# Kernel tuning notes

Hardware: AMD Instinct MI355X
Metric: run time of the kernel (lower is better)

Reference implementation:

```python
import jax, jax.numpy as jnp
import numpy as np

B, S, HID = 1, 2048, 4096
NH, NKV, HD = 32, 8, 128          # num_heads, num_key_value_heads, head_dim
N_REP = NH // NKV                  # GQA group size
ROPE_BASE = 10000.0


def rotate_half(x):
    x1, x2 = jnp.split(x, 2, axis=-1)
    return jnp.concatenate([-x2, x1], axis=-1)


def setup_inputs() -> dict:
    key = jax.random.key(0)
    k_hs, k_q, k_k, k_v, k_o = jax.random.split(key, 5)
    hidden_states = jax.random.normal(k_hs, (B, S, HID), dtype=jnp.float32)
    scale = 0.02
    wq = jax.random.normal(k_q, (HID, NH * HD), dtype=jnp.float32) * scale
    wk = jax.random.normal(k_k, (HID, NKV * HD), dtype=jnp.float32) * scale
    wv = jax.random.normal(k_v, (HID, NKV * HD), dtype=jnp.float32) * scale
    wo = jax.random.normal(k_o, (NH * HD, HID), dtype=jnp.float32) * scale
    # additive causal mask, 0 on/below diagonal, large negative above
    causal = jnp.tril(jnp.ones((S, S), dtype=bool))
    attention_mask = jnp.where(causal, 0.0, -1e9).astype(jnp.float32)[None, None]
    # RoPE cos/sin cache (LlamaRotaryEmbedding)
    inv_freq = 1.0 / (ROPE_BASE ** (jnp.arange(0, HD, 2, dtype=jnp.float32) / HD))
    t = jnp.arange(S, dtype=jnp.float32)
    freqs = jnp.outer(t, inv_freq)                 # [S, HD/2]
    emb = jnp.concatenate([freqs, freqs], axis=-1)  # [S, HD]
    cos, sin = jnp.cos(emb), jnp.sin(emb)
    return {"hidden_states": hidden_states, "attention_mask": attention_mask,
            "wq": wq, "wk": wk, "wv": wv, "wo": wo, "cos": cos, "sin": sin}


def reference(hidden_states, attention_mask, wq, wk, wv, wo, cos, sin):
    b, s, _ = hidden_states.shape
    # projections -> [b, heads, s, head_dim]
    q = (hidden_states @ wq).reshape(b, s, NH, HD).transpose(0, 2, 1, 3)
    k = (hidden_states @ wk).reshape(b, s, NKV, HD).transpose(0, 2, 1, 3)
    v = (hidden_states @ wv).reshape(b, s, NKV, HD).transpose(0, 2, 1, 3)
    # RoPE: cos/sin [s, hd] broadcast over batch and heads
    c = cos[None, None, :, :]
    sn = sin[None, None, :, :]
    q = q * c + rotate_half(q) * sn
    k = k * c + rotate_half(k) * sn
    # GQA repeat_kv: [b, nkv, s, d] -> [b, nh, s, d]
    k = jnp.repeat(k, N_REP, axis=1)
    v = jnp.repeat(v, N_REP, axis=1)
    scores = jnp.einsum('bhqd,bhkd->bhqk', q, k) / jnp.sqrt(jnp.float32(HD))
    scores = scores + attention_mask
    attn = jax.nn.softmax(scores.astype(jnp.float32), axis=-1).astype(q.dtype)
    out = jnp.einsum('bhqk,bhkd->bhqd', attn, v)        # [b, nh, s, d]
    out = out.transpose(0, 2, 1, 3).reshape(b, s, NH * HD)
    return out @ wo
```

## Files before the change

### kernel.cpp

```cpp
#include <hip/hip_runtime.h>


typedef __bf16 bf16_t;
typedef bf16_t bf16x8_t __attribute__((ext_vector_type(8)));
typedef float f32x4_t __attribute__((ext_vector_type(4)));

#define S_LEN 2048
#define HID 4096
#define NH 32
#define NKV 8
#define HD 128
#define KV_DIM 1024
#define QKV_DIM 6144
#define SCALE 0.08838834764831845f

__device__ __align__(16) bf16_t g_hsb[(size_t)S_LEN * HID];
__device__ __align__(16) bf16_t g_wqkvT[(size_t)QKV_DIM * HID];
__device__ __align__(16) bf16_t g_woT[(size_t)HID * HID];
__device__ __align__(16) bf16_t g_qkv[(size_t)S_LEN * QKV_DIM];
__device__ __align__(16) bf16_t g_vT[(size_t)NKV * HD * S_LEN];
__device__ __align__(16) bf16_t g_ao[(size_t)S_LEN * HID];

__device__ __forceinline__ void gl_lds16(const bf16_t* g, bf16_t* l) {
  __builtin_amdgcn_global_load_lds(
      (const __attribute__((address_space(1))) void*)g,
      (__attribute__((address_space(3))) void*)l, 16, 0, 0);
}

__global__ __launch_bounds__(256) void cast_f32_bf16(
    const float* __restrict__ in, bf16_t* __restrict__ out)
{
  size_t i = ((size_t)blockIdx.x * 256 + threadIdx.x) * 8;
  float4 a = *(const float4*)(in + i);
  float4 b = *(const float4*)(in + i + 4);
  bf16x8_t r;
  r[0] = (bf16_t)a.x; r[1] = (bf16_t)a.y; r[2] = (bf16_t)a.z; r[3] = (bf16_t)a.w;
  r[4] = (bf16_t)b.x; r[5] = (bf16_t)b.y; r[6] = (bf16_t)b.z; r[7] = (bf16_t)b.w;
  *(bf16x8_t*)(out + i) = r;
}

__global__ __launch_bounds__(256) void transpose_f32_bf16(
    const float* __restrict__ in, bf16_t* __restrict__ out, int is, int os)
{
  __shared__ __align__(16) bf16_t T[64 * 72];
  int r0 = blockIdx.x * 64, c0 = blockIdx.y * 64;
  int t = threadIdx.x;
#pragma unroll
  for (int it = 0; it < 2; ++it) {
    int idx = t + it * 256;
    int r = idx >> 3, c8 = (idx & 7) * 8;
    const float* p = in + (size_t)(r0 + r) * is + c0 + c8;
    float4 a = *(const float4*)p;
    float4 b = *(const float4*)(p + 4);
    bf16x8_t x;
    x[0] = (bf16_t)a.x; x[1] = (bf16_t)a.y; x[2] = (bf16_t)a.z; x[3] = (bf16_t)a.w;
    x[4] = (bf16_t)b.x; x[5] = (bf16_t)b.y; x[6] = (bf16_t)b.z; x[7] = (bf16_t)b.w;
    *(bf16x8_t*)(T + r * 72 + c8) = x;
  }
  __syncthreads();
#pragma unroll
  for (int it = 0; it < 2; ++it) {
    int idx = t + it * 256;
    int c = idx >> 3, r8 = (idx & 7) * 8;
    bf16x8_t x;
#pragma unroll
    for (int i = 0; i < 8; ++i) x[i] = T[(r8 + i) * 72 + c];
    *(bf16x8_t*)(out + (size_t)(c0 + c) * os + r0 + r8) = x;
  }
}

__global__ __launch_bounds__(256) void transpose_bf16(
    const bf16_t* __restrict__ in, bf16_t* __restrict__ out,
    int is, int os, int in_b, int out_b)
{
  __shared__ __align__(16) bf16_t T[64 * 72];
  const bf16_t* inp = in + (size_t)blockIdx.z * in_b;
  bf16_t* outp = out + (size_t)blockIdx.z * out_b;
  int r0 = blockIdx.x * 64, c0 = blockIdx.y * 64;
  int t = threadIdx.x;
#pragma unroll
  for (int it = 0; it < 2; ++it) {
    int idx = t + it * 256;
    int r = idx >> 3, c8 = (idx & 7) * 8;
    *(bf16x8_t*)(T + r * 72 + c8) =
        *(const bf16x8_t*)(inp + (size_t)(r0 + r) * is + c0 + c8);
  }
  __syncthreads();
#pragma unroll
  for (int it = 0; it < 2; ++it) {
    int idx = t + it * 256;
    int c = idx >> 3, r8 = (idx & 7) * 8;
    bf16x8_t x;
#pragma unroll
    for (int i = 0; i < 8; ++i) x[i] = T[(r8 + i) * 72 + c];
    *(bf16x8_t*)(outp + (size_t)(c0 + c) * os + r0 + r8) = x;
  }
}

template <typename CT>
__global__ __launch_bounds__(256) void gemm128(
    const bf16_t* __restrict__ A, const bf16_t* __restrict__ Bt,
    CT* __restrict__ C, int K, int N)
{
  __shared__ __align__(16) bf16_t As[128 * 32];
  __shared__ __align__(16) bf16_t Bs[128 * 32];
  int t = threadIdx.x;
  int wave = t >> 6, lane = t & 63, ln = lane & 15, lq = lane >> 4;
  int m0 = blockIdx.x * 128, n0 = blockIdx.y * 128;
  int wm = (wave >> 1) * 64, wn = (wave & 1) * 64;
  int srow = wave * 16 + (lane >> 2);
  int skc = (lane & 3) * 8;
  const bf16_t* Ag0 = A + (size_t)(m0 + srow) * K + skc;
  const bf16_t* Ag1 = A + (size_t)(m0 + 64 + srow) * K + skc;
  const bf16_t* Bg0 = Bt + (size_t)(n0 + srow) * K + skc;
  const bf16_t* Bg1 = Bt + (size_t)(n0 + 64 + srow) * K + skc;
  bf16_t* Al0 = As + (wave * 16) * 32;
  bf16_t* Al1 = As + (64 + wave * 16) * 32;
  bf16_t* Bl0 = Bs + (wave * 16) * 32;
  bf16_t* Bl1 = Bs + (64 + wave * 16) * 32;
  f32x4_t acc[4][4] = {};
  for (int k0 = 0; k0 < K; k0 += 32) {
    __syncthreads();
    gl_lds16(Ag0 + k0, Al0);
    gl_lds16(Ag1 + k0, Al1);
    gl_lds16(Bg0 + k0, Bl0);
    gl_lds16(Bg1 + k0, Bl1);
    __syncthreads();
    bf16x8_t af[4], bfr[4];
#pragma unroll
    for (int i = 0; i < 4; ++i) {
      af[i]  = *(const bf16x8_t*)(As + (wm + i * 16 + ln) * 32 + lq * 8);
      bfr[i] = *(const bf16x8_t*)(Bs + (wn + i * 16 + ln) * 32 + lq * 8);
    }
#pragma unroll
    for (int mt = 0; mt < 4; ++mt)
#pragma unroll
      for (int nt = 0; nt < 4; ++nt)
        acc[mt][nt] = __builtin_amdgcn_mfma_f32_16x16x32_bf16(
            af[mt], bfr[nt], acc[mt][nt], 0, 0, 0);
  }
#pragma unroll
  for (int mt = 0; mt < 4; ++mt)
#pragma unroll
    for (int nt = 0; nt < 4; ++nt)
#pragma unroll
      for (int r = 0; r < 4; ++r)
        C[(size_t)(m0 + wm + mt * 16 + lq * 4 + r) * N + n0 + wn + nt * 16 + ln] =
            (CT)acc[mt][nt][r];
}

__global__ __launch_bounds__(256) void rope_kernel(
    bf16_t* __restrict__ qkv, const float* __restrict__ cs,
    const float* __restrict__ sn)
{
  int idx = blockIdx.x * 256 + threadIdx.x;
  int d = idx & 63;
  int h = (idx >> 6) % (NH + NKV);
  int s = idx / (64 * (NH + NKV));
  float c = cs[s * HD + d], si = sn[s * HD + d];
  bf16_t* base = qkv + (size_t)s * QKV_DIM +
                 ((h < NH) ? h * HD : HID + (h - NH) * HD);
  float x1 = (float)base[d], x2 = (float)base[d + 64];
  base[d]      = (bf16_t)(x1 * c - x2 * si);
  base[d + 64] = (bf16_t)(x2 * c + x1 * si);
}

__global__ __launch_bounds__(256) void attn_kernel(
    const bf16_t* __restrict__ QKV, const bf16_t* __restrict__ VT,
    bf16_t* __restrict__ O)
{
  __shared__ __align__(16) bf16_t Ks[64 * 136];
  __shared__ __align__(16) bf16_t Vs[128 * 72];
  __shared__ __align__(16) bf16_t Ps[4 * 16 * 72];
  int t = threadIdx.x, wave = t >> 6, lane = t & 63;
  int ln = lane & 15, lq = lane >> 4;
  int bid = blockIdx.x;
  int qb = (S_LEN / 64 - 1) - (bid >> 5);
  int head = bid & 31, kvh = head >> 2;
  int q0 = qb * 64;
  int qr = q0 + wave * 16 + ln;

  bf16x8_t qf[4];
#pragma unroll
  for (int kk = 0; kk < 4; ++kk)
    qf[kk] = *(const bf16x8_t*)(QKV + (size_t)qr * QKV_DIM + head * HD +
                                kk * 32 + lq * 8);

  f32x4_t oa[8] = {};
  float m_r[4] = {-1e30f, -1e30f, -1e30f, -1e30f};
  float l_r[4] = {0.f, 0.f, 0.f, 0.f};

  int krow = t >> 4, kdc = (t & 15) * 8;
  int vrow = t >> 3, vkc = (t & 7) * 8;
  const bf16_t* Kg = QKV + HID + (size_t)kvh * HD;
  const bf16_t* Vg = VT + (size_t)kvh * HD * S_LEN;

  for (int kt = 0; kt <= qb; ++kt) {
    int kb = kt * 64;
    __syncthreads();
#pragma unroll
    for (int p = 0; p < 4; ++p) {
      int r_ = p * 16 + krow;
      *(bf16x8_t*)(Ks + r_ * 136 + kdc) =
          *(const bf16x8_t*)(Kg + (size_t)(kb + r_) * QKV_DIM + kdc);
      int d_ = p * 32 + vrow;
      *(bf16x8_t*)(Vs + d_ * 72 + vkc) =
          *(const bf16x8_t*)(Vg + (size_t)d_ * S_LEN + kb + vkc);
    }
    __syncthreads();

    f32x4_t sv[4] = {};
#pragma unroll
    for (int nt = 0; nt < 4; ++nt)
#pragma unroll
      for (int kk = 0; kk < 4; ++kk) {
        bf16x8_t kf = *(const bf16x8_t*)(Ks + (nt * 16 + ln) * 136 +
                                         kk * 32 + lq * 8);
        sv[nt] = __builtin_amdgcn_mfma_f32_16x16x32_bf16(qf[kk], kf, sv[nt],
                                                         0, 0, 0);
      }

    float p_[4][4];
    if (kt == qb) {
#pragma unroll
      for (int nt = 0; nt < 4; ++nt)
#pragma unroll
        for (int r = 0; r < 4; ++r) {
          int rq = wave * 16 + lq * 4 + r;
          p_[nt][r] = (nt * 16 + ln <= rq) ? sv[nt][r] * SCALE : -1e30f;
        }
    } else {
#pragma unroll
      for (int nt = 0; nt < 4; ++nt)
#pragma unroll
        for (int r = 0; r < 4; ++r) p_[nt][r] = sv[nt][r] * SCALE;
    }

    float mx[4];
#pragma unroll
    for (int r = 0; r < 4; ++r)
      mx[r] = fmaxf(fmaxf(p_[0][r], p_[1][r]), fmaxf(p_[2][r], p_[3][r]));
#pragma unroll
    for (int off = 8; off >= 1; off >>= 1)
#pragma unroll
      for (int r = 0; r < 4; ++r) mx[r] = fmaxf(mx[r], __shfl_xor(mx[r], off, 64));

    float al[4], rs[4];
#pragma unroll
    for (int r = 0; r < 4; ++r) {
      float mn = fmaxf(m_r[r], mx[r]);
      al[r] = __expf(m_r[r] - mn);
      m_r[r] = mn;
      rs[r] = 0.f;
#pragma unroll
      for (int nt = 0; nt < 4; ++nt) {
        p_[nt][r] = __expf(p_[nt][r] - mn);
        rs[r] += p_[nt][r];
      }
    }
#pragma unroll
    for (int off = 8; off >= 1; off >>= 1)
#pragma unroll
      for (int r = 0; r < 4; ++r) rs[r] += __shfl_xor(rs[r], off, 64);
#pragma unroll
    for (int r = 0; r < 4; ++r) l_r[r] = l_r[r] * al[r] + rs[r];
#pragma unroll
    for (int dt = 0; dt < 8; ++dt)
#pragma unroll
      for (int r = 0; r < 4; ++r) oa[dt][r] *= al[r];

    bf16_t* myP = Ps + wave * 16 * 72;
#pragma unroll
    for (int nt = 0; nt < 4; ++nt)
#pragma unroll
      for (int r = 0; r < 4; ++r)
        myP[(lq * 4 + r) * 72 + nt * 16 + ln] = (bf16_t)p_[nt][r];
    bf16x8_t pf0 = *(const bf16x8_t*)(myP + ln * 72 + lq * 8);
    bf16x8_t pf1 = *(const bf16x8_t*)(myP + ln * 72 + 32 + lq * 8);
#pragma unroll
    for (int dt = 0; dt < 8; ++dt) {
      bf16x8_t v0 = *(const bf16x8_t*)(Vs + (dt * 16 + ln) * 72 + lq * 8);
      bf16x8_t v1 = *(const bf16x8_t*)(Vs + (dt * 16 + ln) * 72 + 32 + lq * 8);
      oa[dt] = __builtin_amdgcn_mfma_f32_16x16x32_bf16(pf0, v0, oa[dt], 0, 0, 0);
      oa[dt] = __builtin_amdgcn_mfma_f32_16x16x32_bf16(pf1, v1, oa[dt], 0, 0, 0);
    }
  }

#pragma unroll
  for (int dt = 0; dt < 8; ++dt)
#pragma unroll
    for (int r = 0; r < 4; ++r) {
      int row = q0 + wave * 16 + lq * 4 + r;
      O[(size_t)row * HID + head * HD + dt * 16 + ln] =
          (bf16_t)(oa[dt][r] / l_r[r]);
    }
}

extern "C" void kernel_launch(void* const* d_in, const int* in_sizes, int n_in,
                              void* d_out, int out_size, void* d_ws, size_t ws_size,
                              hipStream_t stream)
{
  (void)in_sizes; (void)n_in; (void)out_size; (void)d_ws; (void)ws_size;
  const float* hs = (const float*)d_in[0];
  const float* wq = (const float*)d_in[2];
  const float* wk = (const float*)d_in[3];
  const float* wv = (const float*)d_in[4];
  const float* wo = (const float*)d_in[5];
  const float* cs = (const float*)d_in[6];
  const float* sn = (const float*)d_in[7];
  float* out = (float*)d_out;

  bf16_t *hsb, *wqkvT, *woT, *qkv, *vT, *ao;
  hipGetSymbolAddress((void**)&hsb,   HIP_SYMBOL(g_hsb));
  hipGetSymbolAddress((void**)&wqkvT, HIP_SYMBOL(g_wqkvT));
  hipGetSymbolAddress((void**)&woT,   HIP_SYMBOL(g_woT));
  hipGetSymbolAddress((void**)&qkv,   HIP_SYMBOL(g_qkv));
  hipGetSymbolAddress((void**)&vT,    HIP_SYMBOL(g_vT));
  hipGetSymbolAddress((void**)&ao,    HIP_SYMBOL(g_ao));

  cast_f32_bf16<<<(S_LEN * HID) / (256 * 8), 256, 0, stream>>>(hs, hsb);

  transpose_f32_bf16<<<dim3(64, 64), 256, 0, stream>>>(wq, wqkvT, HID, HID);
  transpose_f32_bf16<<<dim3(64, 16), 256, 0, stream>>>(
      wk, wqkvT + (size_t)HID * HID, KV_DIM, HID);
  transpose_f32_bf16<<<dim3(64, 16), 256, 0, stream>>>(
      wv, wqkvT + (size_t)(HID + KV_DIM) * HID, KV_DIM, HID);
  transpose_f32_bf16<<<dim3(64, 64), 256, 0, stream>>>(wo, woT, HID, HID);

  gemm128<bf16_t><<<dim3(S_LEN / 128, QKV_DIM / 128), 256, 0, stream>>>(
      hsb, wqkvT, qkv, HID, QKV_DIM);

  rope_kernel<<<(S_LEN * (NH + NKV) * 64) / 256, 256, 0, stream>>>(qkv, cs, sn);

  transpose_bf16<<<dim3(S_LEN / 64, HD / 64, NKV), 256, 0, stream>>>(
      qkv + HID + KV_DIM, vT, QKV_DIM, S_LEN, HD, HD * S_LEN);

  attn_kernel<<<dim3((S_LEN / 64) * NH), 256, 0, stream>>>(qkv, vT, ao);

  gemm128<float><<<dim3(S_LEN / 128, HID / 128), 256, 0, stream>>>(
      ao, woT, out, HID, HID);
}
```

Before: 672.8 us.

## Replace GEMM with 8-wave 128x256 triple-buffered swizzled LDS pipeline

Rewrites both projection GEMMs as an 8-wave, 128x256-tile kernel with K-step 64. Global-to-LDS loads are triple-buffered and issued two tiles ahead, and LDS addresses use an XOR swizzle to avoid bank conflicts. MFMA phases are interleaved with staged loads using barriers and setprio. The aim is to hide memory latency and raise MFMA utilisation over the old single-buffered 128x128 kernel. In exchange it uses more LDS (144KB) and more registers, which limits occupancy, and it relies on careful manual vmcnt accounting.

```diff
diff --git a/kernel.cpp b/kernel.cpp
--- a/kernel.cpp
+++ b/kernel.cpp
@@ -98,55 +98,117 @@
 }
 
 template <typename CT>
-__global__ __launch_bounds__(256) void gemm128(
+__global__ __launch_bounds__(512, 2) void gemm8p(
     const bf16_t* __restrict__ A, const bf16_t* __restrict__ Bt,
     CT* __restrict__ C, int K, int N)
 {
-  __shared__ __align__(16) bf16_t As[128 * 32];
-  __shared__ __align__(16) bf16_t Bs[128 * 32];
-  int t = threadIdx.x;
-  int wave = t >> 6, lane = t & 63, ln = lane & 15, lq = lane >> 4;
-  int m0 = blockIdx.x * 128, n0 = blockIdx.y * 128;
-  int wm = (wave >> 1) * 64, wn = (wave & 1) * 64;
-  int srow = wave * 16 + (lane >> 2);
-  int skc = (lane & 3) * 8;
-  const bf16_t* Ag0 = A + (size_t)(m0 + srow) * K + skc;
-  const bf16_t* Ag1 = A + (size_t)(m0 + 64 + srow) * K + skc;
-  const bf16_t* Bg0 = Bt + (size_t)(n0 + srow) * K + skc;
-  const bf16_t* Bg1 = Bt + (size_t)(n0 + 64 + srow) * K + skc;
-  bf16_t* Al0 = As + (wave * 16) * 32;
-  bf16_t* Al1 = As + (64 + wave * 16) * 32;
-  bf16_t* Bl0 = Bs + (wave * 16) * 32;
-  bf16_t* Bl1 = Bs + (64 + wave * 16) * 32;
+  constexpr int BM = 128, BN = 256;
+  constexpr int BUFE = (BM + BN) * 64;
+  __shared__ __align__(16) bf16_t lds[3 * BUFE];
+  const int t = threadIdx.x;
+  const int wid = t >> 6, lane = t & 63;
+  const int ln = lane & 15, lq = lane >> 4;
+  const int wm = wid >> 2, wn = wid & 3;
+  const int m0 = blockIdx.x * BM, n0 = blockIdx.y * BN;
+
+  const int lane_xor = (ln & 4) << 3;
+  const int abase = (((wm * 64 + ln) * 128 + lq * 16) ^ lane_xor);
+  const int bbase = (((wn * 64 + ln) * 128 + lq * 16) ^ lane_xor);
+
+  const int srow = t >> 3;
+  const int scol = ((((t & 7) * 16) ^ ((srow & 4) << 3)) >> 1);
+  const bf16_t* Ag0 = A + (size_t)(m0 + srow) * K + scol;
+  const bf16_t* Ag1 = Ag0 + (size_t)64 * K;
+  const bf16_t* Bg0 = Bt + (size_t)(n0 + srow) * K + scol;
+  const bf16_t* Bg1 = Bg0 + (size_t)64 * K;
+  const bf16_t* Bg2 = Bg0 + (size_t)128 * K;
+  const bf16_t* Bg3 = Bg0 + (size_t)192 * K;
+  const int swb = wid * 512;
+
+  {
+    bf16_t* Lb = lds + swb;
+    gl_lds16(Ag0, Lb);            gl_lds16(Ag1, Lb + 4096);
+    gl_lds16(Bg0, Lb + 8192);     gl_lds16(Bg1, Lb + 12288);
+    gl_lds16(Bg2, Lb + 16384);    gl_lds16(Bg3, Lb + 20480);
+    Lb = lds + BUFE + swb;
+    gl_lds16(Ag0 + 64, Lb);         gl_lds16(Ag1 + 64, Lb + 4096);
+    gl_lds16(Bg0 + 64, Lb + 8192);  gl_lds16(Bg1 + 64, Lb + 12288);
+    gl_lds16(Bg2 + 64, Lb + 16384); gl_lds16(Bg3 + 64, Lb + 20480);
+  }
+  asm volatile("s_waitcnt vmcnt(6)" ::: "memory");
+  __builtin_amdgcn_sched_barrier(0);
+  __builtin_amdgcn_s_barrier();
+
   f32x4_t acc[4][4] = {};
-  for (int k0 = 0; k0 < K; k0 += 32) {
-    __syncthreads();
-    gl_lds16(Ag0 + k0, Al0);
-    gl_lds16(Ag1 + k0, Al1);
-    gl_lds16(Bg0 + k0, Bl0);
-    gl_lds16(Bg1 + k0, Bl1);
-    __syncthreads();
+  const int NT = K >> 6;
+  for (int tt = 0; tt < NT; ++tt) {
+    const char* Rb = (const char*)(lds + (tt % 3) * BUFE);
+    const char* Bb = Rb + 16384;
+    bf16_t* Ls = lds + ((tt + 2) % 3) * BUFE + swb;
+    const int k2 = (tt + 2) << 6;
+    const bool stg = (tt + 2) < NT;
     bf16x8_t af[4], bfr[4];
-#pragma unroll
-    for (int i = 0; i < 4; ++i) {
-      af[i]  = *(const bf16x8_t*)(As + (wm + i * 16 + ln) * 32 + lq * 8);
-      bfr[i] = *(const bf16x8_t*)(Bs + (wn + i * 16 + ln) * 32 + lq * 8);
-    }
-#pragma unroll
-    for (int mt = 0; mt < 4; ++mt)
-#pragma unroll
-      for (int nt = 0; nt < 4; ++nt)
-        acc[mt][nt] = __builtin_amdgcn_mfma_f32_16x16x32_bf16(
-            af[mt], bfr[nt], acc[mt][nt], 0, 0, 0);
-  }
-#pragma unroll
-  for (int mt = 0; mt < 4; ++mt)
-#pragma unroll
-    for (int nt = 0; nt < 4; ++nt)
+
+#pragma unroll
+    for (int mi = 0; mi < 4; ++mi)
+      af[mi] = *(const bf16x8_t*)(Rb + abase + mi * 2048);
+#pragma unroll
+    for (int ni = 0; ni < 4; ++ni)
+      bfr[ni] = *(const bf16x8_t*)(Bb + bbase + ni * 2048);
+    if (stg) {
+      gl_lds16(Ag0 + k2, Ls);
+      gl_lds16(Ag1 + k2, Ls + 4096);
+      gl_lds16(Bg0 + k2, Ls + 8192);
+    }
+    __builtin_amdgcn_s_barrier();
+    __builtin_amdgcn_s_setprio(1);
+#pragma unroll
+    for (int mi = 0; mi < 4; ++mi)
+#pragma unroll
+      for (int ni = 0; ni < 4; ++ni)
+        acc[mi][ni] = __builtin_amdgcn_mfma_f32_16x16x32_bf16(
+            af[mi], bfr[ni], acc[mi][ni], 0, 0, 0);
+    __builtin_amdgcn_s_setprio(0);
+    __builtin_amdgcn_s_barrier();
+
+#pragma unroll
+    for (int mi = 0; mi < 4; ++mi)
+      af[mi] = *(const bf16x8_t*)(Rb + abase + mi * 2048 + 64);
+#pragma unroll
+    for (int ni = 0; ni < 4; ++ni)
+      bfr[ni] = *(const bf16x8_t*)(Bb + bbase + ni * 2048 + 64);
+    if (stg) {
+      gl_lds16(Bg1 + k2, Ls + 12288);
+      gl_lds16(Bg2 + k2, Ls + 16384);
+      gl_lds16(Bg3 + k2, Ls + 20480);
+    }
+    __builtin_amdgcn_s_barrier();
+    __builtin_amdgcn_s_setprio(1);
+#pragma unroll
+    for (int mi = 0; mi < 4; ++mi)
+#pragma unroll
+      for (int ni = 0; ni < 4; ++ni)
+        acc[mi][ni] = __builtin_amdgcn_mfma_f32_16x16x32_bf16(
+            af[mi], bfr[ni], acc[mi][ni], 0, 0, 0);
+    __builtin_amdgcn_s_setprio(0);
+
+    if (tt + 2 < NT) {
+      asm volatile("s_waitcnt vmcnt(6)" ::: "memory");
+    } else {
+      asm volatile("s_waitcnt vmcnt(0)" ::: "memory");
+    }
+    __builtin_amdgcn_sched_barrier(0);
+    __builtin_amdgcn_s_barrier();
+  }
+
+#pragma unroll
+  for (int mi = 0; mi < 4; ++mi)
+#pragma unroll
+    for (int ni = 0; ni < 4; ++ni)
 #pragma unroll
       for (int r = 0; r < 4; ++r)
-        C[(size_t)(m0 + wm + mt * 16 + lq * 4 + r) * N + n0 + wn + nt * 16 + ln] =
-            (CT)acc[mt][nt][r];
+        C[(size_t)(m0 + wm * 64 + mi * 16 + lq * 4 + r) * N
+          + n0 + wn * 64 + ni * 16 + ln] = (CT)acc[mi][ni][r];
 }
 
 __global__ __launch_bounds__(256) void rope_kernel(
@@ -327,7 +389,7 @@
       wv, wqkvT + (size_t)(HID + KV_DIM) * HID, KV_DIM, HID);
   transpose_f32_bf16<<<dim3(64, 64), 256, 0, stream>>>(wo, woT, HID, HID);
 
-  gemm128<bf16_t><<<dim3(S_LEN / 128, QKV_DIM / 128), 256, 0, stream>>>(
+  gemm8p<bf16_t><<<dim3(S_LEN / 128, QKV_DIM / 256), 512, 0, stream>>>(
       hsb, wqkvT, qkv, HID, QKV_DIM);
 
   rope_kernel<<<(S_LEN * (NH + NKV) * 64) / 256, 256, 0, stream>>>(qkv, cs, sn);
@@ -337,6 +399,6 @@
 
   attn_kernel<<<dim3((S_LEN / 64) * NH), 256, 0, stream>>>(qkv, vT, ao);
 
-  gemm128<float><<<dim3(S_LEN / 128, HID / 128), 256, 0, stream>>>(
+  gemm8p<float><<<dim3(S_LEN / 128, HID / 256), 512, 0, stream>>>(
       ao, woT, out, HID, HID);
 }
```

Measured after the change: 605.0 us. 10.1% less time.

## Replace 128x128 GEMM with 256x256 double-buffered, swizzled, pipelined MFMA GEMM

Applied to the files above, without the earlier changes.

Replaces the simple 128x128 tile GEMM, which syncs twice per 32-wide K step, with a 256x256 tile, 512-thread kernel. It double-buffers 64-wide K slabs in LDS, XOR-swizzles LDS columns to avoid bank conflicts, interleaves async global-to-LDS staging with MFMA phases using explicit vmcnt waits, and raises wave priority around the MFMAs. The aim is more reuse per loaded byte and hiding memory latency behind compute in both projection GEMMs. In exchange it uses 128KB of LDS and many accumulator registers, and it launches fewer blocks (e.g. 128 for the output projection), which may underfill the device.

```diff
diff --git a/kernel.cpp b/kernel.cpp
--- a/kernel.cpp
+++ b/kernel.cpp
@@ -97,56 +97,108 @@
   }
 }
 
+#define VM4 asm volatile("s_waitcnt vmcnt(4)" ::: "memory")
+#define VM0 asm volatile("s_waitcnt vmcnt(0)" ::: "memory")
+#define SCHB __builtin_amdgcn_sched_barrier(0)
+#define SBAR __builtin_amdgcn_s_barrier()
+
+#define STAGE_A(tau, h)                                                     \
+  { bf16_t* d_ = lds + (((tau) & 1) << 15) + (h) * 8192 + swb;              \
+    const bf16_t* g_ = Ags + (size_t)((h) * 128) * K + (tau) * 64;          \
+    gl_lds16(g_, d_); gl_lds16(g_ + (size_t)64 * K, d_ + 4096); }
+#define STAGE_B(tau, h)                                                     \
+  { bf16_t* d_ = lds + (((tau) & 1) << 15) + 16384 + (h) * 8192 + swb;      \
+    const bf16_t* g_ = Bgs + (size_t)((h) * 128) * K + (tau) * 64;          \
+    gl_lds16(g_, d_); gl_lds16(g_ + (size_t)64 * K, d_ + 4096); }
+
+#define GPHASE(BUF, Q, STAGES, ENDSYNC)                                     \
+  {                                                                         \
+    if ((Q) == 0) {                                                         \
+      _Pragma("unroll")                                                     \
+      for (int ni = 0; ni < 4; ++ni) {                                      \
+        bq[ni][0] = *(const bf16x8_t*)((BUF) + boff + ni * 2048 + colb0);   \
+        bq[ni][1] = *(const bf16x8_t*)((BUF) + boff + ni * 2048 + colb1);   \
+      }                                                                     \
+    }                                                                       \
+    bf16x8_t a00 = *(const bf16x8_t*)((BUF) + aoff + (2*(Q)) * 2048 + colb0);   \
+    bf16x8_t a01 = *(const bf16x8_t*)((BUF) + aoff + (2*(Q)) * 2048 + colb1);   \
+    bf16x8_t a10 = *(const bf16x8_t*)((BUF) + aoff + (2*(Q)+1) * 2048 + colb0); \
+    bf16x8_t a11 = *(const bf16x8_t*)((BUF) + aoff + (2*(Q)+1) * 2048 + colb1); \
+    STAGES;                                                                 \
+    SBAR;                                                                   \
+    asm volatile("s_waitcnt lgkmcnt(0)" ::: "memory");                      \
+    SCHB;                                                                   \
+    __builtin_amdgcn_s_setprio(1);                                          \
+    _Pragma("unroll")                                                       \
+    for (int ni = 0; ni < 4; ++ni) {                                        \
+      acc[2*(Q)][ni]   = __builtin_amdgcn_mfma_f32_16x16x32_bf16(a00, bq[ni][0], acc[2*(Q)][ni],   0, 0, 0); \
+      acc[2*(Q)][ni]   = __builtin_amdgcn_mfma_f32_16x16x32_bf16(a01, bq[ni][1], acc[2*(Q)][ni],   0, 0, 0); \
+      acc[2*(Q)+1][ni] = __builtin_amdgcn_mfma_f32_16x16x32_bf16(a10, bq[ni][0], acc[2*(Q)+1][ni], 0, 0, 0); \
+      acc[2*(Q)+1][ni] = __builtin_amdgcn_mfma_f32_16x16x32_bf16(a11, bq[ni][1], acc[2*(Q)+1][ni], 0, 0, 0); \
+    }                                                                       \
+    __builtin_amdgcn_s_setprio(0);                                          \
+    ENDSYNC;                                                                \
+  }
+
 template <typename CT>
-__global__ __launch_bounds__(256) void gemm128(
+__global__ __launch_bounds__(512, 2) void gemm256(
     const bf16_t* __restrict__ A, const bf16_t* __restrict__ Bt,
     CT* __restrict__ C, int K, int N)
 {
-  __shared__ __align__(16) bf16_t As[128 * 32];
-  __shared__ __align__(16) bf16_t Bs[128 * 32];
-  int t = threadIdx.x;
-  int wave = t >> 6, lane = t & 63, ln = lane & 15, lq = lane >> 4;
-  int m0 = blockIdx.x * 128, n0 = blockIdx.y * 128;
-  int wm = (wave >> 1) * 64, wn = (wave & 1) * 64;
-  int srow = wave * 16 + (lane >> 2);
-  int skc = (lane & 3) * 8;
-  const bf16_t* Ag0 = A + (size_t)(m0 + srow) * K + skc;
-  const bf16_t* Ag1 = A + (size_t)(m0 + 64 + srow) * K + skc;
-  const bf16_t* Bg0 = Bt + (size_t)(n0 + srow) * K + skc;
-  const bf16_t* Bg1 = Bt + (size_t)(n0 + 64 + srow) * K + skc;
-  bf16_t* Al0 = As + (wave * 16) * 32;
-  bf16_t* Al1 = As + (64 + wave * 16) * 32;
-  bf16_t* Bl0 = Bs + (wave * 16) * 32;
-  bf16_t* Bl1 = Bs + (64 + wave * 16) * 32;
-  f32x4_t acc[4][4] = {};
-  for (int k0 = 0; k0 < K; k0 += 32) {
-    __syncthreads();
-    gl_lds16(Ag0 + k0, Al0);
-    gl_lds16(Ag1 + k0, Al1);
-    gl_lds16(Bg0 + k0, Bl0);
-    gl_lds16(Bg1 + k0, Bl1);
-    __syncthreads();
-    bf16x8_t af[4], bfr[4];
-#pragma unroll
-    for (int i = 0; i < 4; ++i) {
-      af[i]  = *(const bf16x8_t*)(As + (wm + i * 16 + ln) * 32 + lq * 8);
-      bfr[i] = *(const bf16x8_t*)(Bs + (wn + i * 16 + ln) * 32 + lq * 8);
-    }
-#pragma unroll
-    for (int mt = 0; mt < 4; ++mt)
-#pragma unroll
-      for (int nt = 0; nt < 4; ++nt)
-        acc[mt][nt] = __builtin_amdgcn_mfma_f32_16x16x32_bf16(
-            af[mt], bfr[nt], acc[mt][nt], 0, 0, 0);
-  }
-#pragma unroll
-  for (int mt = 0; mt < 4; ++mt)
-#pragma unroll
-    for (int nt = 0; nt < 4; ++nt)
+  __shared__ __align__(16) bf16_t lds[2 * 32768];
+  const int t = threadIdx.x;
+  const int wid = t >> 6, lane = t & 63;
+  const int ln = lane & 15, lq = lane >> 4;
+  const int wm = wid >> 2, wn = wid & 3;
+  const int m0 = blockIdx.x * 256, n0 = blockIdx.y * 256;
+
+  const int lx = (ln & 7) << 4;
+  const int colb0 = (lq * 16) ^ lx;
+  const int colb1 = (64 + lq * 16) ^ lx;
+  const int aoff = wm * 16384 + ln * 128;
+  const int boff = 32768 + (wn >> 1) * 16384 + ((wn & 1) * 64 + ln) * 128;
+
+  const int srow = t >> 3;
+  const int scol = ((((t & 7) * 16) ^ ((srow & 7) << 4)) >> 1);
+  const int swb = wid * 512;
+  const bf16_t* Ags = A + (size_t)(m0 + srow) * K + scol;
+  const bf16_t* Bgs = Bt + (size_t)(n0 + srow) * K + scol;
+
+  f32x4_t acc[8][4] = {};
+  bf16x8_t bq[4][2];
+  const char* const bufE = (const char*)lds;
+  const char* const bufO = (const char*)lds + 65536;
+  const int NITER = K >> 7;
+
+  STAGE_A(0, 0) STAGE_A(0, 1) STAGE_B(0, 0) STAGE_B(0, 1)
+  STAGE_B(1, 0) STAGE_B(1, 1)
+  VM4;
+  SCHB;
+  SBAR;
+
+  for (int I = 0; I < NITER; ++I) {
+    const bool stg = (I + 1 < NITER);
+    const int tb = 2 * I;
+    GPHASE(bufE, 0, STAGE_A(tb + 1, 0), SBAR)
+    GPHASE(bufE, 1, STAGE_A(tb + 1, 1), SBAR)
+    GPHASE(bufE, 2, if (stg) STAGE_B(tb + 2, 0), SBAR)
+    GPHASE(bufE, 3, if (stg) STAGE_B(tb + 2, 1),
+           { if (stg) { VM4; } else { VM0; } SCHB; SBAR; })
+    GPHASE(bufO, 0, if (stg) STAGE_A(tb + 2, 0), SBAR)
+    GPHASE(bufO, 1, if (stg) STAGE_A(tb + 2, 1), SBAR)
+    GPHASE(bufO, 2, if (stg) STAGE_B(tb + 3, 0), SBAR)
+    GPHASE(bufO, 3, if (stg) STAGE_B(tb + 3, 1),
+           { if (stg) { VM4; SCHB; } SBAR; })
+  }
+
+#pragma unroll
+  for (int mi = 0; mi < 8; ++mi)
+#pragma unroll
+    for (int ni = 0; ni < 4; ++ni)
 #pragma unroll
       for (int r = 0; r < 4; ++r)
-        C[(size_t)(m0 + wm + mt * 16 + lq * 4 + r) * N + n0 + wn + nt * 16 + ln] =
-            (CT)acc[mt][nt][r];
+        C[(size_t)(m0 + wm * 128 + mi * 16 + lq * 4 + r) * N
+          + n0 + wn * 64 + ni * 16 + ln] = (CT)acc[mi][ni][r];
 }
 
 __global__ __launch_bounds__(256) void rope_kernel(
@@ -327,7 +379,7 @@
       wv, wqkvT + (size_t)(HID + KV_DIM) * HID, KV_DIM, HID);
   transpose_f32_bf16<<<dim3(64, 64), 256, 0, stream>>>(wo, woT, HID, HID);
 
-  gemm128<bf16_t><<<dim3(S_LEN / 128, QKV_DIM / 128), 256, 0, stream>>>(
+  gemm256<bf16_t><<<dim3(S_LEN / 256, QKV_DIM / 256), 512, 0, stream>>>(
       hsb, wqkvT, qkv, HID, QKV_DIM);
 
   rope_kernel<<<(S_LEN * (NH + NKV) * 64) / 256, 256, 0, stream>>>(qkv, cs, sn);
@@ -337,6 +389,6 @@
 
   attn_kernel<<<dim3((S_LEN / 64) * NH), 256, 0, stream>>>(qkv, vT, ao);
 
-  gemm128<float><<<dim3(S_LEN / 128, HID / 128), 256, 0, stream>>>(
+  gemm256<float><<<dim3(S_LEN / 256, HID / 256), 512, 0, stream>>>(
       ao, woT, out, HID, HID);
 }
```

Result: faster. 589.6 us (-12.4%).
